# Kernel tuning notes

Hardware: AMD Instinct MI355X
Metric: run time of the kernel (lower is better)

Reference implementation:

```python
import jax, jax.numpy as jnp
import numpy as np

NUM_NODES = 8192
IN_FEATURES = 1024
OUT_FEATURES = 512
NUM_EDGES = 262144  # avg degree 32


def setup_inputs() -> dict:
    key = jax.random.key(0)
    k_x, k_w, k_b, k_src, k_dst = jax.random.split(key, 5)
    x = jax.random.normal(k_x, (NUM_NODES, IN_FEATURES), dtype=jnp.float32)
    # torch nn.Linear layout: weight [out, in], bias [out]
    W = jax.random.normal(k_w, (OUT_FEATURES, IN_FEATURES), dtype=jnp.float32) * (1.0 / np.sqrt(IN_FEATURES))
    b = jax.random.normal(k_b, (OUT_FEATURES,), dtype=jnp.float32) * 0.01
    src = jax.random.randint(k_src, (NUM_EDGES,), 0, NUM_NODES, dtype=jnp.int64)
    dst = jax.random.randint(k_dst, (NUM_EDGES,), 0, NUM_NODES, dtype=jnp.int64)
    edge_index = jnp.stack([src, dst], axis=0)
    return {"x": x, "W": W, "b": b, "edge_index": edge_index, "num_nodes": NUM_NODES}


def reference(x, W, b, edge_index, num_nodes):
    # Faithful to the torch module: build dense adjacency from edge list
    # (duplicate edges collapse to 1.0 via assignment semantics),
    # linear, (dropout p=0 -> identity), dense adj @ hidden, relu.
    adj = jnp.zeros((num_nodes, num_nodes), dtype=x.dtype)
    adj = adj.at[edge_index[0], edge_index[1]].set(1.0)
    hidden = x @ W.T + b            # [N, out]
    support = adj @ hidden          # [N, out] aggregation over neighbors
    return jax.nn.relu(support)
```

## Files before the change

kernel.cpp:

```cpp
#include <hip/hip_runtime.h>

#define N_NODES 8192
#define IN_F    1024
#define OUT_F   512
#define N_EDGES 262144
#define STRIDE  96

#define HID_OFF     0u
#define XB_OFF      8388608u
#define WB_OFF      25165824u
#define DEG_OFF     26214400u
#define COL_OFF     26247168u
#define MAX_DEG     STRIDE

typedef short  bf16x8 __attribute__((ext_vector_type(8)));
typedef float  f32x4  __attribute__((ext_vector_type(4)));

__device__ __forceinline__ unsigned short f2bf(float f) {
    unsigned u = __float_as_uint(f);
    u += 0x7fffu + ((u >> 16) & 1u);
    return (unsigned short)(u >> 16);
}

__device__ __forceinline__ float bflo(unsigned u) { return __uint_as_float(u << 16); }
__device__ __forceinline__ float bfhi(unsigned u) { return __uint_as_float(u & 0xffff0000u); }

__device__ __forceinline__ void ld_lds16(const void* g, void* l) {
    __builtin_amdgcn_global_load_lds(
        (const __attribute__((address_space(1))) void*)g,
        (__attribute__((address_space(3))) void*)l, 16, 0, 0);
}

#define NX8 (N_NODES * IN_F / 8)
#define NW8 (OUT_F * IN_F / 8)
#define SCAT_BLOCKS 1024
__global__ __launch_bounds__(256) void cvt_scatter(const float* __restrict__ x,
                                                   const float* __restrict__ w,
                                                   unsigned short* __restrict__ xb,
                                                   const int* __restrict__ src,
                                                   const int* __restrict__ dst,
                                                   int* __restrict__ deg,
                                                   int* __restrict__ col) {
    const int bid = blockIdx.x;
    if (bid < SCAT_BLOCKS) {
        int e = bid * 256 + threadIdx.x;
        int s = src[e];
        int slot = atomicAdd(&deg[s], 1);
        if (slot < STRIDE) col[s * STRIDE + slot] = dst[e];
        return;
    }
    int i = (bid - SCAT_BLOCKS) * 256 + threadIdx.x;
    if (i >= NX8 + NW8) return;
    const f32x4* p = (i < NX8) ? ((const f32x4*)x + (size_t)i * 2)
                               : ((const f32x4*)w + (size_t)(i - NX8) * 2);
    f32x4 v0 = __builtin_nontemporal_load(p);
    f32x4 v1 = __builtin_nontemporal_load(p + 1);
    uint4 o;
    o.x = (unsigned)f2bf(v0.x) | ((unsigned)f2bf(v0.y) << 16);
    o.y = (unsigned)f2bf(v0.z) | ((unsigned)f2bf(v0.w) << 16);
    o.z = (unsigned)f2bf(v1.x) | ((unsigned)f2bf(v1.y) << 16);
    o.w = (unsigned)f2bf(v1.z) | ((unsigned)f2bf(v1.w) << 16);
    *((uint4*)xb + i) = o;
}

__global__ __launch_bounds__(256, 2) void gemm(const unsigned short* __restrict__ Xb,
                                               const unsigned short* __restrict__ Wb,
                                               const float* __restrict__ bias,
                                               unsigned short* __restrict__ H) {
    __shared__ unsigned short As[2][128 * 64];
    __shared__ unsigned short Bs[2][64 * 64];

    const int bid = blockIdx.x;
    const int tid = threadIdx.x;
    const int lane = tid & 63;
    const int wave = tid >> 6;
    const int row0 = (bid & 63) * 128;
    const int col0 = (bid >> 6) * 64;
    const int wm   = (wave & 1) * 64;
    const int wn   = (wave >> 1) * 32;
    const int fm   = lane & 15;
    const int fm7  = fm & 7;
    const int q    = lane >> 4;

    f32x4 acc[4][2];
#pragma unroll
    for (int i = 0; i < 4; ++i)
#pragma unroll
        for (int j = 0; j < 2; ++j) acc[i][j] = (f32x4)0.f;

    const int r0 = tid >> 3;
    const int kp = ((tid & 7) ^ (r0 & 7)) * 8;
    const unsigned short* Xbase = Xb + (size_t)(row0 + r0) * IN_F + kp;
    const unsigned short* Wbase = Wb + (size_t)(col0 + r0) * IN_F + kp;

#define STAGE(buf, k0) do {                                                   \
    ld_lds16(Xbase            + (k0), &As[buf][tid * 8]);                     \
    ld_lds16(Xbase + 32*IN_F  + (k0), &As[buf][(tid + 256) * 8]);             \
    ld_lds16(Xbase + 64*IN_F  + (k0), &As[buf][(tid + 512) * 8]);             \
    ld_lds16(Xbase + 96*IN_F  + (k0), &As[buf][(tid + 768) * 8]);             \
    ld_lds16(Wbase            + (k0), &Bs[buf][tid * 8]);                     \
    ld_lds16(Wbase + 32*IN_F  + (k0), &Bs[buf][(tid + 256) * 8]);             \
} while (0)

#define COMPUTE(buf) do {                                                     \
    _Pragma("unroll")                                                         \
    for (int s = 0; s < 2; ++s) {                                             \
        const int kq = s * 4 + q;                                             \
        bf16x8 a[4], b[2];                                                    \
        _Pragma("unroll")                                                     \
        for (int mi = 0; mi < 4; ++mi)                                        \
            a[mi] = *(const bf16x8*)&As[buf][(((wm + mi*16 + fm) << 3) + (kq ^ fm7)) << 3]; \
        _Pragma("unroll")                                                     \
        for (int ni = 0; ni < 2; ++ni)                                        \
            b[ni] = *(const bf16x8*)&Bs[buf][(((wn + ni*16 + fm) << 3) + (kq ^ fm7)) << 3]; \
        _Pragma("unroll")                                                     \
        for (int mi = 0; mi < 4; ++mi)                                        \
            _Pragma("unroll")                                                 \
            for (int ni = 0; ni < 2; ++ni)                                    \
                acc[mi][ni] = __builtin_amdgcn_mfma_f32_16x16x32_bf16(        \
                    a[mi], b[ni], acc[mi][ni], 0, 0, 0);                      \
    }                                                                         \
} while (0)

    STAGE(0, 0);
    __syncthreads();
    int cur = 0;
    for (int t = 0; t < 15; ++t) {
        STAGE(cur ^ 1, (t + 1) * 64);
        COMPUTE(cur);
        __syncthreads();
        cur ^= 1;
    }
    COMPUTE(cur);

    const int cm = (lane >> 4) * 4;
#pragma unroll
    for (int ni = 0; ni < 2; ++ni) {
        const int c = col0 + wn + ni * 16 + fm;
        const float bv = bias[c];
#pragma unroll
        for (int mi = 0; mi < 4; ++mi) {
#pragma unroll
            for (int r = 0; r < 4; ++r) {
                const int row = row0 + wm + mi * 16 + cm + r;
                H[(size_t)row * OUT_F + c] = f2bf(acc[mi][ni][r] + bv);
            }
        }
    }
#undef STAGE
#undef COMPUTE
}

__global__ __launch_bounds__(256, 4) void aggregate(const unsigned short* __restrict__ H,
                                                    const int* __restrict__ dg,
                                                    const int* __restrict__ col,
                                                    float* __restrict__ out) {
    __shared__ int nbr[4][MAX_DEG];
    __shared__ int uniq[4][MAX_DEG];
    __shared__ int wcnt[4];
    const int wave = threadIdx.x >> 6;
    const int lane = threadIdx.x & 63;
    const int v    = blockIdx.x * 4 + wave;
    int d = dg[v];
    if (d > MAX_DEG) d = MAX_DEG;

    if (lane == 0) wcnt[wave] = 0;
    int id0 = -1, id1 = -1;
    if (lane < d)      { id0 = col[v * STRIDE + lane];      nbr[wave][lane]      = id0; }
    if (64 + lane < d) { id1 = col[v * STRIDE + 64 + lane]; nbr[wave][64 + lane] = id1; }
    __builtin_amdgcn_wave_barrier();

    bool k0 = (lane < d);
    const int lim0 = k0 ? lane : 0;
    for (int j = 0; j < lim0; ++j) k0 = k0 & (nbr[wave][j] != id0);
    bool k1 = (64 + lane < d);
    const int lim1 = k1 ? (64 + lane) : 0;
    for (int j = 0; j < lim1; ++j) k1 = k1 & (nbr[wave][j] != id1);
    if (k0) uniq[wave][atomicAdd(&wcnt[wave], 1)] = id0;
    if (k1) uniq[wave][atomicAdd(&wcnt[wave], 1)] = id1;
    __builtin_amdgcn_wave_barrier();
    const int n  = wcnt[wave];
    const int f0 = lane * 8;
    const int* uq = &uniq[wave][0];

    float a0=0,a1=0,a2=0,a3=0,a4=0,a5=0,a6=0,a7=0;
    int e = 0;
    for (; e + 16 <= n; e += 16) {
        uint4 h[16];
#pragma unroll
        for (int t = 0; t < 16; ++t)
            h[t] = *(const uint4*)&H[(size_t)uq[e + t] * OUT_F + f0];
#pragma unroll
        for (int t = 0; t < 16; ++t) {
            a0 += bflo(h[t].x); a1 += bfhi(h[t].x);
            a2 += bflo(h[t].y); a3 += bfhi(h[t].y);
            a4 += bflo(h[t].z); a5 += bfhi(h[t].z);
            a6 += bflo(h[t].w); a7 += bfhi(h[t].w);
        }
    }
    for (; e + 4 <= n; e += 4) {
        uint4 h[4];
#pragma unroll
        for (int t = 0; t < 4; ++t)
            h[t] = *(const uint4*)&H[(size_t)uq[e + t] * OUT_F + f0];
#pragma unroll
        for (int t = 0; t < 4; ++t) {
            a0 += bflo(h[t].x); a1 += bfhi(h[t].x);
            a2 += bflo(h[t].y); a3 += bfhi(h[t].y);
            a4 += bflo(h[t].z); a5 += bfhi(h[t].z);
            a6 += bflo(h[t].w); a7 += bfhi(h[t].w);
        }
    }
    for (; e < n; ++e) {
        uint4 h0 = *(const uint4*)&H[(size_t)uq[e] * OUT_F + f0];
        a0 += bflo(h0.x); a1 += bfhi(h0.x);
        a2 += bflo(h0.y); a3 += bfhi(h0.y);
        a4 += bflo(h0.z); a5 += bfhi(h0.z);
        a6 += bflo(h0.w); a7 += bfhi(h0.w);
    }
    f32x4 o0 = {fmaxf(a0,0.f), fmaxf(a1,0.f), fmaxf(a2,0.f), fmaxf(a3,0.f)};
    f32x4 o1 = {fmaxf(a4,0.f), fmaxf(a5,0.f), fmaxf(a6,0.f), fmaxf(a7,0.f)};
    __builtin_nontemporal_store(o0, (f32x4*)&out[(size_t)v * OUT_F + f0]);
    __builtin_nontemporal_store(o1, (f32x4*)&out[(size_t)v * OUT_F + f0 + 4]);
}

extern "C" void kernel_launch(void* const* d_in, const int* in_sizes, int n_in,
                              void* d_out, int out_size, void* d_ws, size_t ws_size,
                              hipStream_t stream) {
    const float* x  = (const float*)d_in[0];
    const float* W  = (const float*)d_in[1];
    const float* b  = (const float*)d_in[2];
    const int*   ei = (const int*)d_in[3];
    float* out = (float*)d_out;

    char* ws = (char*)d_ws;
    unsigned short* H   = (unsigned short*)(ws + HID_OFF);
    unsigned short* Xb  = (unsigned short*)(ws + XB_OFF);
    unsigned short* Wb  = (unsigned short*)(ws + WB_OFF);
    int*            deg = (int*)(ws + DEG_OFF);
    int*            col = (int*)(ws + COL_OFF);

    hipMemsetAsync(deg, 0, N_NODES * sizeof(int), stream);

    cvt_scatter<<<SCAT_BLOCKS + (NX8 + NW8) / 256, 256, 0, stream>>>(
        x, W, Xb, ei, ei + N_EDGES, deg, col);

    gemm<<<512, 256, 0, stream>>>(Xb, Wb, b, H);

    aggregate<<<N_NODES / 4, 256, 0, stream>>>(H, deg, col, out);
}
```

Measured before the change: 147.8 us.

## Fuse scatter/convert, GEMM and aggregation into one persistent kernel with grid barriers

Replaces the three kernel launches with a single persistent kernel of 512 blocks. The blocks synchronise between phases through an atomic-counter grid barrier, and the barrier counters are cleared by the existing memset. The aim is to remove launch gaps and tail effects between kernels. In exchange, the aggregation phase now runs with only 512 blocks doing 4 rounds each at occupancy 2, so it has less parallelism. The grid barrier also relies on all 512 blocks being co-resident.

```diff
diff --git a/kernel.cpp b/kernel.cpp
--- a/kernel.cpp
+++ b/kernel.cpp
@@ -5,13 +5,17 @@
 #define OUT_F   512
 #define N_EDGES 262144
 #define STRIDE  96
+#define MAX_DEG STRIDE
+
+#define GRID     512
+#define NTHREADS (GRID * 256)
 
 #define HID_OFF     0u
 #define XB_OFF      8388608u
 #define WB_OFF      25165824u
 #define DEG_OFF     26214400u
-#define COL_OFF     26247168u
-#define MAX_DEG     STRIDE
+#define BAR_OFF     26247168u
+#define COL_OFF     26247424u
 
 typedef short  bf16x8 __attribute__((ext_vector_type(8)));
 typedef float  f32x4  __attribute__((ext_vector_type(4)));
@@ -31,88 +35,111 @@
         (__attribute__((address_space(3))) void*)l, 16, 0, 0);
 }
 
+__device__ __forceinline__ void gbar(int* cnt) {
+    __syncthreads();
+    if (threadIdx.x == 0) {
+        __threadfence();
+        __hip_atomic_fetch_add(cnt, 1, __ATOMIC_ACQ_REL, __HIP_MEMORY_SCOPE_AGENT);
+        while (__hip_atomic_load(cnt, __ATOMIC_ACQUIRE, __HIP_MEMORY_SCOPE_AGENT) < GRID)
+            __builtin_amdgcn_s_sleep(1);
+        __threadfence();
+    }
+    __syncthreads();
+}
+
 #define NX8 (N_NODES * IN_F / 8)
 #define NW8 (OUT_F * IN_F / 8)
-#define SCAT_BLOCKS 1024
-__global__ __launch_bounds__(256) void cvt_scatter(const float* __restrict__ x,
-                                                   const float* __restrict__ w,
-                                                   unsigned short* __restrict__ xb,
-                                                   const int* __restrict__ src,
-                                                   const int* __restrict__ dst,
-                                                   int* __restrict__ deg,
-                                                   int* __restrict__ col) {
-    const int bid = blockIdx.x;
-    if (bid < SCAT_BLOCKS) {
-        int e = bid * 256 + threadIdx.x;
-        int s = src[e];
-        int slot = atomicAdd(&deg[s], 1);
-        if (slot < STRIDE) col[s * STRIDE + slot] = dst[e];
-        return;
-    }
-    int i = (bid - SCAT_BLOCKS) * 256 + threadIdx.x;
-    if (i >= NX8 + NW8) return;
-    const f32x4* p = (i < NX8) ? ((const f32x4*)x + (size_t)i * 2)
-                               : ((const f32x4*)w + (size_t)(i - NX8) * 2);
-    f32x4 v0 = __builtin_nontemporal_load(p);
-    f32x4 v1 = __builtin_nontemporal_load(p + 1);
-    uint4 o;
-    o.x = (unsigned)f2bf(v0.x) | ((unsigned)f2bf(v0.y) << 16);
-    o.y = (unsigned)f2bf(v0.z) | ((unsigned)f2bf(v0.w) << 16);
-    o.z = (unsigned)f2bf(v1.x) | ((unsigned)f2bf(v1.y) << 16);
-    o.w = (unsigned)f2bf(v1.z) | ((unsigned)f2bf(v1.w) << 16);
-    *((uint4*)xb + i) = o;
-}
-
-__global__ __launch_bounds__(256, 2) void gemm(const unsigned short* __restrict__ Xb,
-                                               const unsigned short* __restrict__ Wb,
-                                               const float* __restrict__ bias,
-                                               unsigned short* __restrict__ H) {
-    __shared__ unsigned short As[2][128 * 64];
-    __shared__ unsigned short Bs[2][64 * 64];
-
-    const int bid = blockIdx.x;
-    const int tid = threadIdx.x;
+
+__global__ __launch_bounds__(256, 2) void fused(const float* __restrict__ x,
+                                                const float* __restrict__ w,
+                                                const float* __restrict__ bias,
+                                                const int* __restrict__ src,
+                                                const int* __restrict__ dst,
+                                                unsigned short* __restrict__ Xb,
+                                                unsigned short* __restrict__ Wb,
+                                                unsigned short* __restrict__ H,
+                                                int* __restrict__ deg,
+                                                int* __restrict__ col,
+                                                int* __restrict__ bar,
+                                                float* __restrict__ out) {
+    __shared__ unsigned long long smem8[49152 / 8];
+    unsigned short* As0 = (unsigned short*)smem8;
+    unsigned short* Bs0 = As0 + 2 * 128 * 64;
+
+    const int bid  = blockIdx.x;
+    const int tid  = threadIdx.x;
     const int lane = tid & 63;
     const int wave = tid >> 6;
-    const int row0 = (bid & 63) * 128;
-    const int col0 = (bid >> 6) * 64;
-    const int wm   = (wave & 1) * 64;
-    const int wn   = (wave >> 1) * 32;
-    const int fm   = lane & 15;
-    const int fm7  = fm & 7;
-    const int q    = lane >> 4;
-
-    f32x4 acc[4][2];
-#pragma unroll
-    for (int i = 0; i < 4; ++i)
-#pragma unroll
-        for (int j = 0; j < 2; ++j) acc[i][j] = (f32x4)0.f;
-
-    const int r0 = tid >> 3;
-    const int kp = ((tid & 7) ^ (r0 & 7)) * 8;
-    const unsigned short* Xbase = Xb + (size_t)(row0 + r0) * IN_F + kp;
-    const unsigned short* Wbase = Wb + (size_t)(col0 + r0) * IN_F + kp;
+
+    {
+        const int e0 = bid * 256 + tid;
+        const int e1 = e0 + NTHREADS;
+        const int s0 = src[e0], d0 = dst[e0];
+        const int s1 = src[e1], d1 = dst[e1];
+        int sl0 = atomicAdd(&deg[s0], 1);
+        if (sl0 < STRIDE) col[s0 * STRIDE + sl0] = d0;
+        int sl1 = atomicAdd(&deg[s1], 1);
+        if (sl1 < STRIDE) col[s1 * STRIDE + sl1] = d1;
+
+        for (int i = e0; i < NX8 + NW8; i += NTHREADS) {
+            const f32x4* p = (i < NX8) ? ((const f32x4*)x + (size_t)i * 2)
+                                       : ((const f32x4*)w + (size_t)(i - NX8) * 2);
+            f32x4 v0 = __builtin_nontemporal_load(p);
+            f32x4 v1 = __builtin_nontemporal_load(p + 1);
+            uint4 o;
+            o.x = (unsigned)f2bf(v0.x) | ((unsigned)f2bf(v0.y) << 16);
+            o.y = (unsigned)f2bf(v0.z) | ((unsigned)f2bf(v0.w) << 16);
+            o.z = (unsigned)f2bf(v1.x) | ((unsigned)f2bf(v1.y) << 16);
+            o.w = (unsigned)f2bf(v1.z) | ((unsigned)f2bf(v1.w) << 16);
+            *((uint4*)Xb + i) = o;
+        }
+    }
+    gbar(&bar[0]);
+
+    {
+        const int row0 = (bid & 63) * 128;
+        const int col0 = (bid >> 6) * 64;
+        const int wm   = (wave & 1) * 64;
+        const int wn   = (wave >> 1) * 32;
+        const int fm   = lane & 15;
+        const int fm7  = fm & 7;
+        const int q    = lane >> 4;
+
+        f32x4 acc[4][2];
+#pragma unroll
+        for (int i = 0; i < 4; ++i)
+#pragma unroll
+            for (int j = 0; j < 2; ++j) acc[i][j] = (f32x4)0.f;
+
+        const int r0 = tid >> 3;
+        const int kp = ((tid & 7) ^ (r0 & 7)) * 8;
+        const unsigned short* Xbase = Xb + (size_t)(row0 + r0) * IN_F + kp;
+        const unsigned short* Wbase = Wb + (size_t)(col0 + r0) * IN_F + kp;
 
 #define STAGE(buf, k0) do {                                                   \
-    ld_lds16(Xbase            + (k0), &As[buf][tid * 8]);                     \
-    ld_lds16(Xbase + 32*IN_F  + (k0), &As[buf][(tid + 256) * 8]);             \
-    ld_lds16(Xbase + 64*IN_F  + (k0), &As[buf][(tid + 512) * 8]);             \
-    ld_lds16(Xbase + 96*IN_F  + (k0), &As[buf][(tid + 768) * 8]);             \
-    ld_lds16(Wbase            + (k0), &Bs[buf][tid * 8]);                     \
-    ld_lds16(Wbase + 32*IN_F  + (k0), &Bs[buf][(tid + 256) * 8]);             \
+    unsigned short* A_ = As0 + (buf) * (128 * 64);                            \
+    unsigned short* B_ = Bs0 + (buf) * (64 * 64);                             \
+    ld_lds16(Xbase            + (k0), A_ + tid * 8);                          \
+    ld_lds16(Xbase + 32*IN_F  + (k0), A_ + (tid + 256) * 8);                  \
+    ld_lds16(Xbase + 64*IN_F  + (k0), A_ + (tid + 512) * 8);                  \
+    ld_lds16(Xbase + 96*IN_F  + (k0), A_ + (tid + 768) * 8);                  \
+    ld_lds16(Wbase            + (k0), B_ + tid * 8);                          \
+    ld_lds16(Wbase + 32*IN_F  + (k0), B_ + (tid + 256) * 8);                  \
 } while (0)
 
 #define COMPUTE(buf) do {                                                     \
+    const unsigned short* A_ = As0 + (buf) * (128 * 64);                      \
+    const unsigned short* B_ = Bs0 + (buf) * (64 * 64);                       \
     _Pragma("unroll")                                                         \
     for (int s = 0; s < 2; ++s) {                                             \
         const int kq = s * 4 + q;                                             \
         bf16x8 a[4], b[2];                                                    \
         _Pragma("unroll")                                                     \
         for (int mi = 0; mi < 4; ++mi)                                        \
-            a[mi] = *(const bf16x8*)&As[buf][(((wm + mi*16 + fm) << 3) + (kq ^ fm7)) << 3]; \
+            a[mi] = *(const bf16x8*)&A_[(((wm + mi*16 + fm) << 3) + (kq ^ fm7)) << 3]; \
         _Pragma("unroll")                                                     \
         for (int ni = 0; ni < 2; ++ni)                                        \
-            b[ni] = *(const bf16x8*)&Bs[buf][(((wn + ni*16 + fm) << 3) + (kq ^ fm7)) << 3]; \
+            b[ni] = *(const bf16x8*)&B_[(((wn + ni*16 + fm) << 3) + (kq ^ fm7)) << 3]; \
         _Pragma("unroll")                                                     \
         for (int mi = 0; mi < 4; ++mi)                                        \
             _Pragma("unroll")                                                 \
@@ -122,106 +149,107 @@
     }                                                                         \
 } while (0)
 
-    STAGE(0, 0);
-    __syncthreads();
-    int cur = 0;
-    for (int t = 0; t < 15; ++t) {
-        STAGE(cur ^ 1, (t + 1) * 64);
+        STAGE(0, 0);
+        __syncthreads();
+        int cur = 0;
+        for (int t = 0; t < 15; ++t) {
+            STAGE(cur ^ 1, (t + 1) * 64);
+            COMPUTE(cur);
+            __syncthreads();
+            cur ^= 1;
+        }
         COMPUTE(cur);
-        __syncthreads();
-        cur ^= 1;
-    }
-    COMPUTE(cur);
-
-    const int cm = (lane >> 4) * 4;
-#pragma unroll
-    for (int ni = 0; ni < 2; ++ni) {
-        const int c = col0 + wn + ni * 16 + fm;
-        const float bv = bias[c];
-#pragma unroll
-        for (int mi = 0; mi < 4; ++mi) {
-#pragma unroll
-            for (int r = 0; r < 4; ++r) {
-                const int row = row0 + wm + mi * 16 + cm + r;
-                H[(size_t)row * OUT_F + c] = f2bf(acc[mi][ni][r] + bv);
-            }
-        }
-    }
+
+        const int cm = (lane >> 4) * 4;
+#pragma unroll
+        for (int ni = 0; ni < 2; ++ni) {
+            const int c = col0 + wn + ni * 16 + fm;
+            const float bv = bias[c];
+#pragma unroll
+            for (int mi = 0; mi < 4; ++mi) {
+#pragma unroll
+                for (int r = 0; r < 4; ++r) {
+                    const int row = row0 + wm + mi * 16 + cm + r;
+                    H[(size_t)row * OUT_F + c] = f2bf(acc[mi][ni][r] + bv);
+                }
+            }
+        }
 #undef STAGE
 #undef COMPUTE
-}
-
-__global__ __launch_bounds__(256, 4) void aggregate(const unsigned short* __restrict__ H,
-                                                    const int* __restrict__ dg,
-                                                    const int* __restrict__ col,
-                                                    float* __restrict__ out) {
-    __shared__ int nbr[4][MAX_DEG];
-    __shared__ int uniq[4][MAX_DEG];
-    __shared__ int wcnt[4];
-    const int wave = threadIdx.x >> 6;
-    const int lane = threadIdx.x & 63;
-    const int v    = blockIdx.x * 4 + wave;
-    int d = dg[v];
-    if (d > MAX_DEG) d = MAX_DEG;
-
-    if (lane == 0) wcnt[wave] = 0;
-    int id0 = -1, id1 = -1;
-    if (lane < d)      { id0 = col[v * STRIDE + lane];      nbr[wave][lane]      = id0; }
-    if (64 + lane < d) { id1 = col[v * STRIDE + 64 + lane]; nbr[wave][64 + lane] = id1; }
-    __builtin_amdgcn_wave_barrier();
-
-    bool k0 = (lane < d);
-    const int lim0 = k0 ? lane : 0;
-    for (int j = 0; j < lim0; ++j) k0 = k0 & (nbr[wave][j] != id0);
-    bool k1 = (64 + lane < d);
-    const int lim1 = k1 ? (64 + lane) : 0;
-    for (int j = 0; j < lim1; ++j) k1 = k1 & (nbr[wave][j] != id1);
-    if (k0) uniq[wave][atomicAdd(&wcnt[wave], 1)] = id0;
-    if (k1) uniq[wave][atomicAdd(&wcnt[wave], 1)] = id1;
-    __builtin_amdgcn_wave_barrier();
-    const int n  = wcnt[wave];
-    const int f0 = lane * 8;
-    const int* uq = &uniq[wave][0];
-
-    float a0=0,a1=0,a2=0,a3=0,a4=0,a5=0,a6=0,a7=0;
-    int e = 0;
-    for (; e + 16 <= n; e += 16) {
-        uint4 h[16];
-#pragma unroll
-        for (int t = 0; t < 16; ++t)
-            h[t] = *(const uint4*)&H[(size_t)uq[e + t] * OUT_F + f0];
-#pragma unroll
-        for (int t = 0; t < 16; ++t) {
-            a0 += bflo(h[t].x); a1 += bfhi(h[t].x);
-            a2 += bflo(h[t].y); a3 += bfhi(h[t].y);
-            a4 += bflo(h[t].z); a5 += bfhi(h[t].z);
-            a6 += bflo(h[t].w); a7 += bfhi(h[t].w);
-        }
-    }
-    for (; e + 4 <= n; e += 4) {
-        uint4 h[4];
-#pragma unroll
-        for (int t = 0; t < 4; ++t)
-            h[t] = *(const uint4*)&H[(size_t)uq[e + t] * OUT_F + f0];
-#pragma unroll
-        for (int t = 0; t < 4; ++t) {
-            a0 += bflo(h[t].x); a1 += bfhi(h[t].x);
-            a2 += bflo(h[t].y); a3 += bfhi(h[t].y);
-            a4 += bflo(h[t].z); a5 += bfhi(h[t].z);
-            a6 += bflo(h[t].w); a7 += bfhi(h[t].w);
-        }
-    }
-    for (; e < n; ++e) {
-        uint4 h0 = *(const uint4*)&H[(size_t)uq[e] * OUT_F + f0];
-        a0 += bflo(h0.x); a1 += bfhi(h0.x);
-        a2 += bflo(h0.y); a3 += bfhi(h0.y);
-        a4 += bflo(h0.z); a5 += bfhi(h0.z);
-        a6 += bflo(h0.w); a7 += bfhi(h0.w);
-    }
-    f32x4 o0 = {fmaxf(a0,0.f), fmaxf(a1,0.f), fmaxf(a2,0.f), fmaxf(a3,0.f)};
-    f32x4 o1 = {fmaxf(a4,0.f), fmaxf(a5,0.f), fmaxf(a6,0.f), fmaxf(a7,0.f)};
-    __builtin_nontemporal_store(o0, (f32x4*)&out[(size_t)v * OUT_F + f0]);
-    __builtin_nontemporal_store(o1, (f32x4*)&out[(size_t)v * OUT_F + f0 + 4]);
+    }
+    gbar(&bar[1]);
+
+    {
+        int* nbr  = (int*)smem8;
+        int* uniq = nbr + 4 * MAX_DEG;
+        int* wcnt = uniq + 4 * MAX_DEG;
+        int* mynbr = nbr  + wave * MAX_DEG;
+        int* myuq  = uniq + wave * MAX_DEG;
+        const int f0 = lane * 8;
+
+        for (int rnd = 0; rnd < 4; ++rnd) {
+            const int v = bid * 16 + wave * 4 + rnd;
+            int d = deg[v];
+            if (d > MAX_DEG) d = MAX_DEG;
+
+            if (lane == 0) wcnt[wave] = 0;
+            int id0 = -1, id1 = -1;
+            if (lane < d)      { id0 = col[v * STRIDE + lane];      mynbr[lane]      = id0; }
+            if (64 + lane < d) { id1 = col[v * STRIDE + 64 + lane]; mynbr[64 + lane] = id1; }
+            __builtin_amdgcn_wave_barrier();
+
+            bool k0 = (lane < d);
+            const int lim0 = k0 ? lane : 0;
+            for (int j = 0; j < lim0; ++j) k0 = k0 & (mynbr[j] != id0);
+            bool k1 = (64 + lane < d);
+            const int lim1 = k1 ? (64 + lane) : 0;
+            for (int j = 0; j < lim1; ++j) k1 = k1 & (mynbr[j] != id1);
+            if (k0) myuq[atomicAdd(&wcnt[wave], 1)] = id0;
+            if (k1) myuq[atomicAdd(&wcnt[wave], 1)] = id1;
+            __builtin_amdgcn_wave_barrier();
+            const int n = wcnt[wave];
+
+            float a0=0,a1=0,a2=0,a3=0,a4=0,a5=0,a6=0,a7=0;
+            int e = 0;
+            for (; e + 16 <= n; e += 16) {
+                uint4 h[16];
+#pragma unroll
+                for (int t = 0; t < 16; ++t)
+                    h[t] = *(const uint4*)&H[(size_t)myuq[e + t] * OUT_F + f0];
+#pragma unroll
+                for (int t = 0; t < 16; ++t) {
+                    a0 += bflo(h[t].x); a1 += bfhi(h[t].x);
+                    a2 += bflo(h[t].y); a3 += bfhi(h[t].y);
+                    a4 += bflo(h[t].z); a5 += bfhi(h[t].z);
+                    a6 += bflo(h[t].w); a7 += bfhi(h[t].w);
+                }
+            }
+            for (; e + 4 <= n; e += 4) {
+                uint4 h[4];
+#pragma unroll
+                for (int t = 0; t < 4; ++t)
+                    h[t] = *(const uint4*)&H[(size_t)myuq[e + t] * OUT_F + f0];
+#pragma unroll
+                for (int t = 0; t < 4; ++t) {
+                    a0 += bflo(h[t].x); a1 += bfhi(h[t].x);
+                    a2 += bflo(h[t].y); a3 += bfhi(h[t].y);
+                    a4 += bflo(h[t].z); a5 += bfhi(h[t].z);
+                    a6 += bflo(h[t].w); a7 += bfhi(h[t].w);
+                }
+            }
+            for (; e < n; ++e) {
+                uint4 h0 = *(const uint4*)&H[(size_t)myuq[e] * OUT_F + f0];
+                a0 += bflo(h0.x); a1 += bfhi(h0.x);
+                a2 += bflo(h0.y); a3 += bfhi(h0.y);
+                a4 += bflo(h0.z); a5 += bfhi(h0.z);
+                a6 += bflo(h0.w); a7 += bfhi(h0.w);
+            }
+            f32x4 o0 = {fmaxf(a0,0.f), fmaxf(a1,0.f), fmaxf(a2,0.f), fmaxf(a3,0.f)};
+            f32x4 o1 = {fmaxf(a4,0.f), fmaxf(a5,0.f), fmaxf(a6,0.f), fmaxf(a7,0.f)};
+            __builtin_nontemporal_store(o0, (f32x4*)&out[(size_t)v * OUT_F + f0]);
+            __builtin_nontemporal_store(o1, (f32x4*)&out[(size_t)v * OUT_F + f0 + 4]);
+        }
+    }
 }
 
 extern "C" void kernel_launch(void* const* d_in, const int* in_sizes, int n_in,
@@ -238,14 +266,11 @@
     unsigned short* Xb  = (unsigned short*)(ws + XB_OFF);
     unsigned short* Wb  = (unsigned short*)(ws + WB_OFF);
     int*            deg = (int*)(ws + DEG_OFF);
+    int*            bar = (int*)(ws + BAR_OFF);
     int*            col = (int*)(ws + COL_OFF);
 
-    hipMemsetAsync(deg, 0, N_NODES * sizeof(int), stream);
-
-    cvt_scatter<<<SCAT_BLOCKS + (NX8 + NW8) / 256, 256, 0, stream>>>(
-        x, W, Xb, ei, ei + N_EDGES, deg, col);
-
-    gemm<<<512, 256, 0, stream>>>(Xb, Wb, b, H);
-
-    aggregate<<<N_NODES / 4, 256, 0, stream>>>(H, deg, col, out);
-}
+    hipMemsetAsync(ws + DEG_OFF, 0, (BAR_OFF - DEG_OFF) + 256, stream);
+
+    fused<<<GRID, 256, 0, stream>>>(x, W, b, ei, ei + N_EDGES,
+                                    Xb, Wb, H, deg, col, bar, out);
+}
```

Measured after the change: 283.8 us. 1.92x slower.

## Fold deg reset into convert, move edge scatter into GEMM, split aggregation by halves

Applied to the files above, without the earlier changes.

Removes the separate memset by zeroing the degree array inside the bf16 conversion kernel. The edge scatter moves out of the conversion launch and runs as extra blocks of the GEMM launch. Aggregation now gives each node to two waves, one per 256-feature half, using 8-byte loads and higher occupancy. In exchange, every wave redoes the neighbor dedup, so that work is duplicated per node.

```diff
diff --git a/kernel.cpp b/kernel.cpp
--- a/kernel.cpp
+++ b/kernel.cpp
@@ -33,23 +33,12 @@
 
 #define NX8 (N_NODES * IN_F / 8)
 #define NW8 (OUT_F * IN_F / 8)
-#define SCAT_BLOCKS 1024
-__global__ __launch_bounds__(256) void cvt_scatter(const float* __restrict__ x,
-                                                   const float* __restrict__ w,
-                                                   unsigned short* __restrict__ xb,
-                                                   const int* __restrict__ src,
-                                                   const int* __restrict__ dst,
-                                                   int* __restrict__ deg,
-                                                   int* __restrict__ col) {
-    const int bid = blockIdx.x;
-    if (bid < SCAT_BLOCKS) {
-        int e = bid * 256 + threadIdx.x;
-        int s = src[e];
-        int slot = atomicAdd(&deg[s], 1);
-        if (slot < STRIDE) col[s * STRIDE + slot] = dst[e];
-        return;
-    }
-    int i = (bid - SCAT_BLOCKS) * 256 + threadIdx.x;
+__global__ __launch_bounds__(256) void cvt_bf16_all(const float* __restrict__ x,
+                                                    const float* __restrict__ w,
+                                                    unsigned short* __restrict__ xb,
+                                                    int* __restrict__ deg) {
+    int i = blockIdx.x * blockDim.x + threadIdx.x;
+    if (i < N_NODES) deg[i] = 0;
     if (i >= NX8 + NW8) return;
     const f32x4* p = (i < NX8) ? ((const f32x4*)x + (size_t)i * 2)
                                : ((const f32x4*)w + (size_t)(i - NX8) * 2);
@@ -63,15 +52,30 @@
     *((uint4*)xb + i) = o;
 }
 
-__global__ __launch_bounds__(256, 2) void gemm(const unsigned short* __restrict__ Xb,
-                                               const unsigned short* __restrict__ Wb,
-                                               const float* __restrict__ bias,
-                                               unsigned short* __restrict__ H) {
+#define GEMM_BLOCKS 512
+
+__global__ __launch_bounds__(256, 2) void gemm_scatter(const unsigned short* __restrict__ Xb,
+                                                       const unsigned short* __restrict__ Wb,
+                                                       const float* __restrict__ bias,
+                                                       unsigned short* __restrict__ H,
+                                                       const int* __restrict__ src,
+                                                       const int* __restrict__ dst,
+                                                       int* __restrict__ deg,
+                                                       int* __restrict__ col) {
     __shared__ unsigned short As[2][128 * 64];
     __shared__ unsigned short Bs[2][64 * 64];
 
     const int bid = blockIdx.x;
     const int tid = threadIdx.x;
+
+    if (bid >= GEMM_BLOCKS) {
+        int e = (bid - GEMM_BLOCKS) * 256 + tid;
+        int s = src[e];
+        int slot = atomicAdd(&deg[s], 1);
+        if (slot < STRIDE) col[s * STRIDE + slot] = dst[e];
+        return;
+    }
+
     const int lane = tid & 63;
     const int wave = tid >> 6;
     const int row0 = (bid & 63) * 128;
@@ -151,7 +155,7 @@
 #undef COMPUTE
 }
 
-__global__ __launch_bounds__(256, 4) void aggregate(const unsigned short* __restrict__ H,
+__global__ __launch_bounds__(256, 8) void aggregate(const unsigned short* __restrict__ H,
                                                     const int* __restrict__ dg,
                                                     const int* __restrict__ col,
                                                     float* __restrict__ out) {
@@ -160,7 +164,9 @@
     __shared__ int wcnt[4];
     const int wave = threadIdx.x >> 6;
     const int lane = threadIdx.x & 63;
-    const int v    = blockIdx.x * 4 + wave;
+    const int task = blockIdx.x * 4 + wave;
+    const int v    = task >> 1;
+    const int half = task & 1;
     int d = dg[v];
     if (d > MAX_DEG) d = MAX_DEG;
 
@@ -180,48 +186,40 @@
     if (k1) uniq[wave][atomicAdd(&wcnt[wave], 1)] = id1;
     __builtin_amdgcn_wave_barrier();
     const int n  = wcnt[wave];
-    const int f0 = lane * 8;
     const int* uq = &uniq[wave][0];
-
-    float a0=0,a1=0,a2=0,a3=0,a4=0,a5=0,a6=0,a7=0;
+    const unsigned short* Hh = H + half * 256 + lane * 4;
+
+    float a0=0,a1=0,a2=0,a3=0;
     int e = 0;
-    for (; e + 16 <= n; e += 16) {
-        uint4 h[16];
-#pragma unroll
-        for (int t = 0; t < 16; ++t)
-            h[t] = *(const uint4*)&H[(size_t)uq[e + t] * OUT_F + f0];
-#pragma unroll
-        for (int t = 0; t < 16; ++t) {
+    for (; e + 12 <= n; e += 12) {
+        uint2 h[12];
+#pragma unroll
+        for (int t = 0; t < 12; ++t)
+            h[t] = *(const uint2*)&Hh[(size_t)uq[e + t] * OUT_F];
+#pragma unroll
+        for (int t = 0; t < 12; ++t) {
             a0 += bflo(h[t].x); a1 += bfhi(h[t].x);
             a2 += bflo(h[t].y); a3 += bfhi(h[t].y);
-            a4 += bflo(h[t].z); a5 += bfhi(h[t].z);
-            a6 += bflo(h[t].w); a7 += bfhi(h[t].w);
         }
     }
     for (; e + 4 <= n; e += 4) {
-        uint4 h[4];
+        uint2 h[4];
 #pragma unroll
         for (int t = 0; t < 4; ++t)
-            h[t] = *(const uint4*)&H[(size_t)uq[e + t] * OUT_F + f0];
+            h[t] = *(const uint2*)&Hh[(size_t)uq[e + t] * OUT_F];
 #pragma unroll
         for (int t = 0; t < 4; ++t) {
             a0 += bflo(h[t].x); a1 += bfhi(h[t].x);
             a2 += bflo(h[t].y); a3 += bfhi(h[t].y);
-            a4 += bflo(h[t].z); a5 += bfhi(h[t].z);
-            a6 += bflo(h[t].w); a7 += bfhi(h[t].w);
         }
     }
     for (; e < n; ++e) {
-        uint4 h0 = *(const uint4*)&H[(size_t)uq[e] * OUT_F + f0];
+        uint2 h0 = *(const uint2*)&Hh[(size_t)uq[e] * OUT_F];
         a0 += bflo(h0.x); a1 += bfhi(h0.x);
         a2 += bflo(h0.y); a3 += bfhi(h0.y);
-        a4 += bflo(h0.z); a5 += bfhi(h0.z);
-        a6 += bflo(h0.w); a7 += bfhi(h0.w);
-    }
-    f32x4 o0 = {fmaxf(a0,0.f), fmaxf(a1,0.f), fmaxf(a2,0.f), fmaxf(a3,0.f)};
-    f32x4 o1 = {fmaxf(a4,0.f), fmaxf(a5,0.f), fmaxf(a6,0.f), fmaxf(a7,0.f)};
-    __builtin_nontemporal_store(o0, (f32x4*)&out[(size_t)v * OUT_F + f0]);
-    __builtin_nontemporal_store(o1, (f32x4*)&out[(size_t)v * OUT_F + f0 + 4]);
+    }
+    f32x4 o = {fmaxf(a0,0.f), fmaxf(a1,0.f), fmaxf(a2,0.f), fmaxf(a3,0.f)};
+    __builtin_nontemporal_store(o, (f32x4*)&out[(size_t)v * OUT_F + half * 256 + lane * 4]);
 }
 
 extern "C" void kernel_launch(void* const* d_in, const int* in_sizes, int n_in,
@@ -240,12 +238,10 @@
     int*            deg = (int*)(ws + DEG_OFF);
     int*            col = (int*)(ws + COL_OFF);
 
-    hipMemsetAsync(deg, 0, N_NODES * sizeof(int), stream);
-
-    cvt_scatter<<<SCAT_BLOCKS + (NX8 + NW8) / 256, 256, 0, stream>>>(
-        x, W, Xb, ei, ei + N_EDGES, deg, col);
-
-    gemm<<<512, 256, 0, stream>>>(Xb, Wb, b, H);
-
-    aggregate<<<N_NODES / 4, 256, 0, stream>>>(H, deg, col, out);
-}
+    cvt_bf16_all<<<(NX8 + NW8 + 255) / 256, 256, 0, stream>>>(x, W, Xb, deg);
+
+    gemm_scatter<<<GEMM_BLOCKS + N_EDGES / 256, 256, 0, stream>>>(
+        Xb, Wb, b, H, ei, ei + N_EDGES, deg, col);
+
+    aggregate<<<N_NODES * 2 / 4, 256, 0, stream>>>(H, deg, col, out);
+}
```

Result: faster. 139.6 us (median of 2 runs) (-5.5%).
